# Kernel optimization log

Hardware: AMD Instinct MI355X
Metric: run time of the kernel (lower is better)

## Reference

```python
import jax, jax.numpy as jnp
import numpy as np

N = 100000          # number of road-network nodes
E = 640000          # number of directed edges (sparse adjacency nnz)
HID = 128           # hidden_dims = lane(16)+type(32)+length(16)+node(64)
N_LAYERS = 3        # hparams.baseline_gat_layer


def setup_inputs() -> dict:
    key = jax.random.key(0)
    ks = jax.random.split(key, 12)
    inp = {
        'node_feature': jax.random.randint(ks[0], (N,), 0, 100000),
        'type_feature': jax.random.randint(ks[1], (N,), 0, 20),
        'length_feature': jax.random.randint(ks[2], (N,), 0, 100),
        'lane_feature': jax.random.randint(ks[3], (N,), 0, 10),
        'adj_src': jax.random.randint(ks[4], (E,), 0, N),
        'adj_dst': jax.random.randint(ks[5], (E,), 0, N),
        'adj_val': jax.random.uniform(ks[6], (E,), dtype=jnp.float32),
        # learned parameters
        'node_emb': jax.random.normal(ks[7], (100000, 64), dtype=jnp.float32) * 0.02,
        'type_emb': jax.random.normal(ks[8], (20, 32), dtype=jnp.float32) * 0.02,
        'length_emb': jax.random.normal(ks[9], (100, 16), dtype=jnp.float32) * 0.02,
        'lane_emb': jax.random.normal(ks[10], (10, 16), dtype=jnp.float32) * 0.02,
        'W': jax.random.normal(ks[11], (HID, HID), dtype=jnp.float32) / np.sqrt(HID),
        'b': jnp.zeros((HID,), dtype=jnp.float32),
    }
    return inp


def spgcn_layer(x, W, b, adj_src, adj_dst, adj_val):
    # GCN layer: out = spmm(adj, x @ W) + b, adj given as COO edge list
    support = x @ W                                # [N, HID]
    msg = support[adj_src] * adj_val[:, None]      # gather + scale, [E, HID]
    agg = jax.ops.segment_sum(msg, adj_dst, num_segments=N)  # scatter-add
    return agg + b


def reference(node_feature, type_feature, length_feature, lane_feature,
              adj_src, adj_dst, adj_val,
              node_emb, type_emb, length_emb, lane_emb, W, b):
    # embedding lookups + concat: [lane, type, length, node] -> [N, HID]
    raw_feat = jnp.concatenate([
        lane_emb[lane_feature],
        type_emb[type_feature],
        length_emb[length_feature],
        node_emb[node_feature],
    ], axis=1)
    # repeated propagation with the SAME shared SPGCN layer weights
    for _ in range(N_LAYERS):
        raw_feat = spgcn_layer(raw_feat, W, b, adj_src, adj_dst, adj_val)
    return raw_feat
```

## Files before the change

### kernel.cpp

```cpp
#include <hip/hip_runtime.h>
#include <hip/hip_bf16.h>

typedef __hip_bfloat16 bf16;
typedef unsigned short ushort_t;
typedef __attribute__((ext_vector_type(8))) short short8;
typedef __attribute__((ext_vector_type(4))) float f32x4;

#define NN 100000
#define NE 640000
#define HD 128
#define NB 391
#define EMB_U 6250
#define PREP_U 64
#define PH0_U (EMB_U + PREP_U + NB)
#define HIST_U 2500
#define GEMM_U 782
#define AGG_U 12500
#define CAST_U 50000
#define LDA 136


__device__ __forceinline__ float bf2f(ushort_t u) {
    unsigned v = (unsigned)u << 16;
    return __builtin_bit_cast(float, v);
}
__device__ __forceinline__ ushort_t f2bf(float f) {
    bf16 h = __float2bfloat16(f);
    return *(ushort_t*)&h;
}

struct P {
    const int *nodef, *typef, *lenf, *lanef, *adj_src, *adj_dst;
    const float *adj_val, *node_emb, *type_emb, *len_emb, *lane_emb, *W, *bias;
    ushort_t *X, *Wt, *SUP;
    int *cnt, *offs, *pos, *bsum;
    int2 *epack;
    float *outf;
    int sup_is_out;
};


__device__ __forceinline__ void embed_unit(int u, int tid, const P& p) {
    const int idx = u * 256 + tid;
    const int i = idx >> 4;
    const int c = (idx & 15) * 8;
    const float* tbl; size_t base;
    if (c < 16)      { tbl = p.lane_emb; base = (size_t)p.lanef[i] * 16 + c; }
    else if (c < 48) { tbl = p.type_emb; base = (size_t)p.typef[i] * 32 + (c - 16); }
    else if (c < 64) { tbl = p.len_emb;  base = (size_t)p.lenf[i]  * 16 + (c - 48); }
    else             { tbl = p.node_emb; base = (size_t)p.nodef[i] * 64 + (c - 64); }
    const float4 f0 = *(const float4*)(tbl + base);
    const float4 f1 = *(const float4*)(tbl + base + 4);
    ushort_t u8[8] = { f2bf(f0.x), f2bf(f0.y), f2bf(f0.z), f2bf(f0.w),
                       f2bf(f1.x), f2bf(f1.y), f2bf(f1.z), f2bf(f1.w) };
    *(uint4*)(p.X + (size_t)i * HD + c) = *(uint4*)u8;
}

__global__ __launch_bounds__(256) void phase0_k(P p) {
    const int v = blockIdx.x;
    const int tid = threadIdx.x;
    if (v < EMB_U) {
        embed_unit(v, tid, p);
    } else if (v < EMB_U + PREP_U) {
        const int idx = (v - EMB_U) * 256 + tid;
        const int n = idx >> 7, k = idx & 127;
        p.Wt[idx] = f2bf(p.W[(size_t)k * HD + n]);
    } else {
        const int idx = (v - EMB_U - PREP_U) * 256 + tid;
        if (idx < NN) p.cnt[idx] = 0;
    }
}


__global__ __launch_bounds__(256) void hist_k(P p) {
    const int e = blockIdx.x * 256 + threadIdx.x;
    atomicAdd(&p.cnt[p.adj_dst[e]], 1);
}

__global__ __launch_bounds__(256) void scan1_k(P p) {
    __shared__ int s[256];
    const int tid = threadIdx.x;
    const int idx = blockIdx.x * 256 + tid;
    s[tid] = (idx < NN) ? p.cnt[idx] : 0;
    __syncthreads();
    for (int o = 128; o; o >>= 1) {
        if (tid < o) s[tid] += s[tid + o];
        __syncthreads();
    }
    if (tid == 0) p.bsum[blockIdx.x] = s[0];
}

__global__ __launch_bounds__(256) void scan3_k(P p) {
    __shared__ int s[256];
    const int b = blockIdx.x;
    const int tid = threadIdx.x;
    int acc = 0;
    for (int i = tid; i < b; i += 256) acc += p.bsum[i];
    s[tid] = acc;
    __syncthreads();
    for (int o = 128; o; o >>= 1) {
        if (tid < o) s[tid] += s[tid + o];
        __syncthreads();
    }
    const int boffv = s[0];
    __syncthreads();
    const int idx = b * 256 + tid;
    int v = (idx < NN) ? p.cnt[idx] : 0;
    s[tid] = v;
    __syncthreads();
    for (int o = 1; o < 256; o <<= 1) {
        int x = (tid >= o) ? s[tid - o] : 0;
        __syncthreads();
        s[tid] += x;
        __syncthreads();
    }
    const int excl = s[tid] - v + boffv;
    if (idx <= NN) {
        p.offs[idx] = excl;
        if (idx < NN) p.pos[idx] = excl;
    }
}

__global__ __launch_bounds__(256) void position_k(P p) {
    const int e = blockIdx.x * 256 + threadIdx.x;
    const int d = p.adj_dst[e];
    const int slot = atomicAdd(&p.pos[d], 1);
    int2 pk;
    pk.x = p.adj_src[e];
    pk.y = __float_as_int(p.adj_val[e]);
    p.epack[slot] = pk;
}


__global__ __launch_bounds__(256) void gemm_k(P p) {
    __shared__ ushort_t Xs[128 * LDA];
    const int tid = threadIdx.x;
    const int row0 = blockIdx.x * 128;
    const ushort_t* __restrict__ X = p.X;

#pragma unroll
    for (int i = 0; i < 8; ++i) {
        int chunk = i * 256 + tid;
        int m = chunk >> 4;
        int c8 = (chunk & 15) * 8;
        int gm = row0 + m;
        if (gm >= NN) gm = NN - 1;
        *(uint4*)&Xs[m * LDA + c8] = *(const uint4*)&X[(size_t)gm * HD + c8];
    }

    const int w = tid >> 6;
    const int ln = tid & 15;
    const int quad = (tid >> 4) & 3;
    const int koff = quad * 8;

    short8 bfrg[2][4];
#pragma unroll
    for (int nt = 0; nt < 2; ++nt)
#pragma unroll
        for (int kc = 0; kc < 4; ++kc)
            bfrg[nt][kc] = *(const short8*)&p.Wt[(size_t)(w * 32 + nt * 16 + ln) * HD + kc * 32 + koff];

    __syncthreads();

    const f32x4 zero = {0.f, 0.f, 0.f, 0.f};
#pragma unroll
    for (int mt = 0; mt < 8; ++mt) {
        short8 afrg[4];
#pragma unroll
        for (int kc = 0; kc < 4; ++kc)
            afrg[kc] = *(const short8*)&Xs[(mt * 16 + ln) * LDA + kc * 32 + koff];
        f32x4 acc[2] = {zero, zero};
#pragma unroll
        for (int nt = 0; nt < 2; ++nt)
#pragma unroll
            for (int kc = 0; kc < 4; ++kc)
                acc[nt] = __builtin_amdgcn_mfma_f32_16x16x32_bf16(
                        afrg[kc], bfrg[nt][kc], acc[nt], 0, 0, 0);
#pragma unroll
        for (int reg = 0; reg < 4; ++reg) {
            int gm = row0 + mt * 16 + quad * 4 + reg;
            if (gm < NN) {
#pragma unroll
                for (int nt = 0; nt < 2; ++nt)
                    p.SUP[(size_t)gm * HD + w * 32 + nt * 16 + ln] = f2bf(acc[nt][reg]);
            }
        }
    }
}

__global__ __launch_bounds__(256) void agg_k(P p, int wout, int skipX) {
    const int node = blockIdx.x * 8 + (threadIdx.x >> 5);
    const int lane = threadIdx.x & 31;
    const int c = lane * 4;
    const int lo = p.offs[node];
    const int hi = p.offs[node + 1];
    const ushort_t* __restrict__ sup = p.SUP;
    float4 a0 = {0,0,0,0}, a1 = {0,0,0,0}, a2 = {0,0,0,0}, a3 = {0,0,0,0};
    int j = lo;
    for (; j + 3 < hi; j += 4) {
        const int2 e0 = p.epack[j], e1 = p.epack[j + 1];
        const int2 e2 = p.epack[j + 2], e3 = p.epack[j + 3];
        const ushort4 u0 = *(const ushort4*)(sup + (size_t)e0.x * HD + c);
        const ushort4 u1 = *(const ushort4*)(sup + (size_t)e1.x * HD + c);
        const ushort4 u2 = *(const ushort4*)(sup + (size_t)e2.x * HD + c);
        const ushort4 u3 = *(const ushort4*)(sup + (size_t)e3.x * HD + c);
        const float v0 = __int_as_float(e0.y), v1 = __int_as_float(e1.y);
        const float v2 = __int_as_float(e2.y), v3 = __int_as_float(e3.y);
        a0.x += bf2f(u0.x)*v0; a0.y += bf2f(u0.y)*v0; a0.z += bf2f(u0.z)*v0; a0.w += bf2f(u0.w)*v0;
        a1.x += bf2f(u1.x)*v1; a1.y += bf2f(u1.y)*v1; a1.z += bf2f(u1.z)*v1; a1.w += bf2f(u1.w)*v1;
        a2.x += bf2f(u2.x)*v2; a2.y += bf2f(u2.y)*v2; a2.z += bf2f(u2.z)*v2; a2.w += bf2f(u2.w)*v2;
        a3.x += bf2f(u3.x)*v3; a3.y += bf2f(u3.y)*v3; a3.z += bf2f(u3.z)*v3; a3.w += bf2f(u3.w)*v3;
    }
    for (; j < hi; ++j) {
        const int2 e0 = p.epack[j];
        const float v0 = __int_as_float(e0.y);
        const ushort4 u0 = *(const ushort4*)(sup + (size_t)e0.x * HD + c);
        a0.x += bf2f(u0.x)*v0; a0.y += bf2f(u0.y)*v0; a0.z += bf2f(u0.z)*v0; a0.w += bf2f(u0.w)*v0;
    }
    const float4 b4 = *(const float4*)(p.bias + c);
    float4 acc;
    acc.x = (a0.x + a1.x) + (a2.x + a3.x) + b4.x;
    acc.y = (a0.y + a1.y) + (a2.y + a3.y) + b4.y;
    acc.z = (a0.z + a1.z) + (a2.z + a3.z) + b4.z;
    acc.w = (a0.w + a1.w) + (a2.w + a3.w) + b4.w;
    const size_t o = (size_t)node * HD + c;
    if (!skipX) {
        ushort4 u; u.x = f2bf(acc.x); u.y = f2bf(acc.y);
        u.z = f2bf(acc.z); u.w = f2bf(acc.w);
        *(ushort4*)(p.X + o) = u;
    }
    if (wout) *(float4*)(p.outf + o) = acc;
}

__global__ __launch_bounds__(256) void cast_k(P p) {
    const int idx = blockIdx.x * 256 + threadIdx.x;
    p.outf[idx] = bf2f(p.X[idx]);
}

extern "C" void kernel_launch(void* const* d_in, const int* in_sizes, int n_in,
                              void* d_out, int out_size, void* d_ws, size_t ws_size,
                              hipStream_t stream) {
    P p;
    p.nodef    = (const int*)d_in[0];
    p.typef    = (const int*)d_in[1];
    p.lenf     = (const int*)d_in[2];
    p.lanef    = (const int*)d_in[3];
    p.adj_src  = (const int*)d_in[4];
    p.adj_dst  = (const int*)d_in[5];
    p.adj_val  = (const float*)d_in[6];
    p.node_emb = (const float*)d_in[7];
    p.type_emb = (const float*)d_in[8];
    p.len_emb  = (const float*)d_in[9];
    p.lane_emb = (const float*)d_in[10];
    p.W        = (const float*)d_in[11];
    p.bias     = (const float*)d_in[12];
    p.outf     = (float*)d_out;

    const size_t xbytes = (size_t)NN * HD * 2;
    char* wp = (char*)d_ws;
    p.X     = (ushort_t*)wp; wp += xbytes;
    p.cnt   = (int*)wp;      wp += (size_t)NN * 4;
    p.offs  = (int*)wp;      wp += 400016;
    p.pos   = (int*)wp;      wp += (size_t)NN * 4;
    p.epack = (int2*)wp;     wp += (size_t)NE * 8;
    p.Wt    = (ushort_t*)wp; wp += 32768;
    p.bsum  = (int*)wp;      wp += 1600;
    const size_t used = (size_t)(wp - (char*)d_ws);
    if (ws_size >= used + xbytes) { p.SUP = (ushort_t*)wp;    p.sup_is_out = 0; }
    else                          { p.SUP = (ushort_t*)d_out; p.sup_is_out = 1; }

    phase0_k<<<PH0_U, 256, 0, stream>>>(p);
    hist_k<<<HIST_U, 256, 0, stream>>>(p);
    scan1_k<<<NB, 256, 0, stream>>>(p);
    scan3_k<<<NB, 256, 0, stream>>>(p);
    position_k<<<HIST_U, 256, 0, stream>>>(p);
    for (int l = 0; l < 3; ++l) {
        gemm_k<<<GEMM_U, 256, 0, stream>>>(p);
        const int wout = (l == 2) && !p.sup_is_out;
        agg_k<<<AGG_U, 256, 0, stream>>>(p, wout, wout);
    }
    if (p.sup_is_out) cast_k<<<CAST_U, 256, 0, stream>>>(p);
}
```

Measured before the change: 351.0 us.

## Reassociate GCN layers: aggregate three times, then apply precomputed W^3

Because the weight is shared and aggregation is linear, the three gemm/aggregate pairs are rewritten as three sparse aggregations of the raw features followed by a single GEMM with W^3. W^2 and W^3 are built in a single-block MFMA kernel, and the bias terms are folded in through the row sums d and A·d times bW and bW². This removes two GEMM passes and the cast fallback, and the final GEMM writes fp32 output directly. In exchange it needs a second bf16 ping-pong buffer and a serial one-block weight kernel, and it changes rounding, since W^3 is stored in bf16.

```diff
diff --git a/kernel.cpp b/kernel.cpp
--- a/kernel.cpp
+++ b/kernel.cpp
@@ -12,11 +12,12 @@
 #define NB 391
 #define EMB_U 6250
 #define PREP_U 64
-#define PH0_U (EMB_U + PREP_U + NB)
+#define CNT_U 391
+#define PH0_U (EMB_U + PREP_U + CNT_U)
 #define HIST_U 2500
 #define GEMM_U 782
 #define AGG_U 12500
-#define CAST_U 50000
+#define D_U 391
 #define LDA 136
 
 
@@ -32,35 +33,31 @@
 struct P {
     const int *nodef, *typef, *lenf, *lanef, *adj_src, *adj_dst;
     const float *adj_val, *node_emb, *type_emb, *len_emb, *lane_emb, *W, *bias;
-    ushort_t *X, *Wt, *SUP;
+    ushort_t *Xa, *Xb, *Wt, *w3t;
+    float *bw, *bw2, *d, *d2;
     int *cnt, *offs, *pos, *bsum;
     int2 *epack;
     float *outf;
-    int sup_is_out;
 };
 
-
-__device__ __forceinline__ void embed_unit(int u, int tid, const P& p) {
-    const int idx = u * 256 + tid;
-    const int i = idx >> 4;
-    const int c = (idx & 15) * 8;
-    const float* tbl; size_t base;
-    if (c < 16)      { tbl = p.lane_emb; base = (size_t)p.lanef[i] * 16 + c; }
-    else if (c < 48) { tbl = p.type_emb; base = (size_t)p.typef[i] * 32 + (c - 16); }
-    else if (c < 64) { tbl = p.len_emb;  base = (size_t)p.lenf[i]  * 16 + (c - 48); }
-    else             { tbl = p.node_emb; base = (size_t)p.nodef[i] * 64 + (c - 64); }
-    const float4 f0 = *(const float4*)(tbl + base);
-    const float4 f1 = *(const float4*)(tbl + base + 4);
-    ushort_t u8[8] = { f2bf(f0.x), f2bf(f0.y), f2bf(f0.z), f2bf(f0.w),
-                       f2bf(f1.x), f2bf(f1.y), f2bf(f1.z), f2bf(f1.w) };
-    *(uint4*)(p.X + (size_t)i * HD + c) = *(uint4*)u8;
-}
 
 __global__ __launch_bounds__(256) void phase0_k(P p) {
     const int v = blockIdx.x;
     const int tid = threadIdx.x;
     if (v < EMB_U) {
-        embed_unit(v, tid, p);
+        const int idx = v * 256 + tid;
+        const int i = idx >> 4;
+        const int c = (idx & 15) * 8;
+        const float* tbl; size_t base;
+        if (c < 16)      { tbl = p.lane_emb; base = (size_t)p.lanef[i] * 16 + c; }
+        else if (c < 48) { tbl = p.type_emb; base = (size_t)p.typef[i] * 32 + (c - 16); }
+        else if (c < 64) { tbl = p.len_emb;  base = (size_t)p.lenf[i]  * 16 + (c - 48); }
+        else             { tbl = p.node_emb; base = (size_t)p.nodef[i] * 64 + (c - 64); }
+        const float4 f0 = *(const float4*)(tbl + base);
+        const float4 f1 = *(const float4*)(tbl + base + 4);
+        ushort_t u8[8] = { f2bf(f0.x), f2bf(f0.y), f2bf(f0.z), f2bf(f0.w),
+                           f2bf(f1.x), f2bf(f1.y), f2bf(f1.z), f2bf(f1.w) };
+        *(uint4*)(p.Xa + (size_t)i * HD + c) = *(uint4*)u8;
     } else if (v < EMB_U + PREP_U) {
         const int idx = (v - EMB_U) * 256 + tid;
         const int n = idx >> 7, k = idx & 127;
@@ -68,6 +65,102 @@
     } else {
         const int idx = (v - EMB_U - PREP_U) * 256 + tid;
         if (idx < NN) p.cnt[idx] = 0;
+    }
+}
+
+__global__ __launch_bounds__(256) void wchain_k(P p) {
+    __shared__ ushort_t WtL[HD * HD];
+    __shared__ ushort_t W2t[HD * HD];
+    const int tid = threadIdx.x;
+    for (int i = tid; i < HD * HD / 8; i += 256)
+        *(uint4*)&WtL[i * 8] = *(const uint4*)&p.Wt[i * 8];
+    __syncthreads();
+
+    const int w = tid >> 6;
+    const int ln = tid & 15;
+    const int quad = (tid >> 4) & 3;
+    const int koff = quad * 8;
+    const f32x4 zero = {0.f, 0.f, 0.f, 0.f};
+
+    short8 bfrg[2][4];
+#pragma unroll
+    for (int nt = 0; nt < 2; ++nt)
+#pragma unroll
+        for (int kc = 0; kc < 4; ++kc)
+            bfrg[nt][kc] = *(const short8*)&WtL[(w * 32 + nt * 16 + ln) * HD + kc * 32 + koff];
+
+#pragma unroll
+    for (int mt = 0; mt < 8; ++mt) {
+        const int m = mt * 16 + ln;
+        short8 afrg[4];
+#pragma unroll
+        for (int kc = 0; kc < 4; ++kc) {
+            ushort_t a[8];
+#pragma unroll
+            for (int j = 0; j < 8; ++j)
+                a[j] = WtL[(kc * 32 + koff + j) * HD + m];
+            afrg[kc] = *(short8*)a;
+        }
+        f32x4 acc[2] = {zero, zero};
+#pragma unroll
+        for (int nt = 0; nt < 2; ++nt)
+#pragma unroll
+            for (int kc = 0; kc < 4; ++kc)
+                acc[nt] = __builtin_amdgcn_mfma_f32_16x16x32_bf16(
+                        afrg[kc], bfrg[nt][kc], acc[nt], 0, 0, 0);
+#pragma unroll
+        for (int nt = 0; nt < 2; ++nt)
+#pragma unroll
+            for (int reg = 0; reg < 4; ++reg) {
+                const int col = w * 32 + nt * 16 + ln;
+                const int row = mt * 16 + quad * 4 + reg;
+                W2t[col * HD + row] = f2bf(acc[nt][reg]);
+            }
+    }
+    __syncthreads();
+
+#pragma unroll
+    for (int mt = 0; mt < 8; ++mt) {
+        const int m = mt * 16 + ln;
+        short8 afrg[4];
+#pragma unroll
+        for (int kc = 0; kc < 4; ++kc) {
+            ushort_t a[8];
+#pragma unroll
+            for (int j = 0; j < 8; ++j)
+                a[j] = W2t[(kc * 32 + koff + j) * HD + m];
+            afrg[kc] = *(short8*)a;
+        }
+        f32x4 acc[2] = {zero, zero};
+#pragma unroll
+        for (int nt = 0; nt < 2; ++nt)
+#pragma unroll
+            for (int kc = 0; kc < 4; ++kc)
+                acc[nt] = __builtin_amdgcn_mfma_f32_16x16x32_bf16(
+                        afrg[kc], bfrg[nt][kc], acc[nt], 0, 0, 0);
+#pragma unroll
+        for (int nt = 0; nt < 2; ++nt)
+#pragma unroll
+            for (int reg = 0; reg < 4; ++reg) {
+                const int col = w * 32 + nt * 16 + ln;
+                const int row = mt * 16 + quad * 4 + reg;
+                p.w3t[col * HD + row] = f2bf(acc[nt][reg]);
+            }
+    }
+    __syncthreads();
+
+    float* bwS = (float*)W2t;
+    if (tid < HD) {
+        float s = 0.f;
+        for (int k = 0; k < HD; ++k) s += p.bias[k] * bf2f(WtL[tid * HD + k]);
+        bwS[tid] = s;
+        p.bw[tid] = s;
+    }
+    __syncthreads();
+    if (tid < HD) {
+        float s = 0.f;
+        for (int k = 0; k < HD; ++k) s += bwS[k] * bf2f(WtL[tid * HD + k]);
+        p.bw2[tid] = s;
     }
 }
 
@@ -131,12 +224,66 @@
     p.epack[slot] = pk;
 }
 
-
-__global__ __launch_bounds__(256) void gemm_k(P p) {
+__global__ __launch_bounds__(256) void agg_k(P p, const ushort_t* __restrict__ Xin,
+                                             ushort_t* __restrict__ Xout, int aux) {
+    if (blockIdx.x >= AGG_U) {
+        const int node = (blockIdx.x - AGG_U) * 256 + threadIdx.x;
+        if (node < NN) {
+            const int lo = p.offs[node], hi = p.offs[node + 1];
+            float s = 0.f;
+            if (aux == 1) {
+                for (int j = lo; j < hi; ++j) s += __int_as_float(p.epack[j].y);
+                p.d[node] = s;
+            } else {
+                for (int j = lo; j < hi; ++j) {
+                    const int2 e = p.epack[j];
+                    s += __int_as_float(e.y) * p.d[e.x];
+                }
+                p.d2[node] = s;
+            }
+        }
+        return;
+    }
+    const int node = blockIdx.x * 8 + (threadIdx.x >> 5);
+    const int lane = threadIdx.x & 31;
+    const int c = lane * 4;
+    const int lo = p.offs[node];
+    const int hi = p.offs[node + 1];
+    float4 a0 = {0,0,0,0}, a1 = {0,0,0,0}, a2 = {0,0,0,0}, a3 = {0,0,0,0};
+    int j = lo;
+    for (; j + 3 < hi; j += 4) {
+        const int2 e0 = p.epack[j], e1 = p.epack[j + 1];
+        const int2 e2 = p.epack[j + 2], e3 = p.epack[j + 3];
+        const ushort4 u0 = *(const ushort4*)(Xin + (size_t)e0.x * HD + c);
+        const ushort4 u1 = *(const ushort4*)(Xin + (size_t)e1.x * HD + c);
+        const ushort4 u2 = *(const ushort4*)(Xin + (size_t)e2.x * HD + c);
+        const ushort4 u3 = *(const ushort4*)(Xin + (size_t)e3.x * HD + c);
+        const float v0 = __int_as_float(e0.y), v1 = __int_as_float(e1.y);
+        const float v2 = __int_as_float(e2.y), v3 = __int_as_float(e3.y);
+        a0.x += bf2f(u0.x)*v0; a0.y += bf2f(u0.y)*v0; a0.z += bf2f(u0.z)*v0; a0.w += bf2f(u0.w)*v0;
+        a1.x += bf2f(u1.x)*v1; a1.y += bf2f(u1.y)*v1; a1.z += bf2f(u1.z)*v1; a1.w += bf2f(u1.w)*v1;
+        a2.x += bf2f(u2.x)*v2; a2.y += bf2f(u2.y)*v2; a2.z += bf2f(u2.z)*v2; a2.w += bf2f(u2.w)*v2;
+        a3.x += bf2f(u3.x)*v3; a3.y += bf2f(u3.y)*v3; a3.z += bf2f(u3.z)*v3; a3.w += bf2f(u3.w)*v3;
+    }
+    for (; j < hi; ++j) {
+        const int2 e0 = p.epack[j];
+        const float v0 = __int_as_float(e0.y);
+        const ushort4 u0 = *(const ushort4*)(Xin + (size_t)e0.x * HD + c);
+        a0.x += bf2f(u0.x)*v0; a0.y += bf2f(u0.y)*v0; a0.z += bf2f(u0.z)*v0; a0.w += bf2f(u0.w)*v0;
+    }
+    float4 acc;
+    acc.x = (a0.x + a1.x) + (a2.x + a3.x);
+    acc.y = (a0.y + a1.y) + (a2.y + a3.y);
+    acc.z = (a0.z + a1.z) + (a2.z + a3.z);
+    acc.w = (a0.w + a1.w) + (a2.w + a3.w);
+    ushort4 u; u.x = f2bf(acc.x); u.y = f2bf(acc.y); u.z = f2bf(acc.z); u.w = f2bf(acc.w);
+    *(ushort4*)(Xout + (size_t)node * HD + c) = u;
+}
+
+__global__ __launch_bounds__(256) void gemmf_k(P p, const ushort_t* __restrict__ X3) {
     __shared__ ushort_t Xs[128 * LDA];
     const int tid = threadIdx.x;
     const int row0 = blockIdx.x * 128;
-    const ushort_t* __restrict__ X = p.X;
 
 #pragma unroll
     for (int i = 0; i < 8; ++i) {
@@ -145,20 +292,26 @@
         int c8 = (chunk & 15) * 8;
         int gm = row0 + m;
         if (gm >= NN) gm = NN - 1;
-        *(uint4*)&Xs[m * LDA + c8] = *(const uint4*)&X[(size_t)gm * HD + c8];
+        *(uint4*)&Xs[m * LDA + c8] = *(const uint4*)&X3[(size_t)gm * HD + c8];
     }
 
     const int w = tid >> 6;
     const int ln = tid & 15;
     const int quad = (tid >> 4) & 3;
     const int koff = quad * 8;
+    const int col0 = w * 32 + ln;
+    const int col1 = col0 + 16;
 
     short8 bfrg[2][4];
 #pragma unroll
     for (int nt = 0; nt < 2; ++nt)
 #pragma unroll
         for (int kc = 0; kc < 4; ++kc)
-            bfrg[nt][kc] = *(const short8*)&p.Wt[(size_t)(w * 32 + nt * 16 + ln) * HD + kc * 32 + koff];
+            bfrg[nt][kc] = *(const short8*)&p.w3t[(size_t)(w * 32 + nt * 16 + ln) * HD + kc * 32 + koff];
+
+    const float bwc0 = p.bw[col0],  bwc1 = p.bw[col1];
+    const float bw2c0 = p.bw2[col0], bw2c1 = p.bw2[col1];
+    const float bc0 = p.bias[col0], bc1 = p.bias[col1];
 
     __syncthreads();
 
@@ -178,63 +331,14 @@
                         afrg[kc], bfrg[nt][kc], acc[nt], 0, 0, 0);
 #pragma unroll
         for (int reg = 0; reg < 4; ++reg) {
-            int gm = row0 + mt * 16 + quad * 4 + reg;
+            const int gm = row0 + mt * 16 + quad * 4 + reg;
             if (gm < NN) {
-#pragma unroll
-                for (int nt = 0; nt < 2; ++nt)
-                    p.SUP[(size_t)gm * HD + w * 32 + nt * 16 + ln] = f2bf(acc[nt][reg]);
+                const float dg = p.d[gm], d2g = p.d2[gm];
+                p.outf[(size_t)gm * HD + col0] = acc[0][reg] + d2g * bw2c0 + dg * bwc0 + bc0;
+                p.outf[(size_t)gm * HD + col1] = acc[1][reg] + d2g * bw2c1 + dg * bwc1 + bc1;
             }
         }
     }
-}
-
-__global__ __launch_bounds__(256) void agg_k(P p, int wout, int skipX) {
-    const int node = blockIdx.x * 8 + (threadIdx.x >> 5);
-    const int lane = threadIdx.x & 31;
-    const int c = lane * 4;
-    const int lo = p.offs[node];
-    const int hi = p.offs[node + 1];
-    const ushort_t* __restrict__ sup = p.SUP;
-    float4 a0 = {0,0,0,0}, a1 = {0,0,0,0}, a2 = {0,0,0,0}, a3 = {0,0,0,0};
-    int j = lo;
-    for (; j + 3 < hi; j += 4) {
-        const int2 e0 = p.epack[j], e1 = p.epack[j + 1];
-        const int2 e2 = p.epack[j + 2], e3 = p.epack[j + 3];
-        const ushort4 u0 = *(const ushort4*)(sup + (size_t)e0.x * HD + c);
-        const ushort4 u1 = *(const ushort4*)(sup + (size_t)e1.x * HD + c);
-        const ushort4 u2 = *(const ushort4*)(sup + (size_t)e2.x * HD + c);
-        const ushort4 u3 = *(const ushort4*)(sup + (size_t)e3.x * HD + c);
-        const float v0 = __int_as_float(e0.y), v1 = __int_as_float(e1.y);
-        const float v2 = __int_as_float(e2.y), v3 = __int_as_float(e3.y);
-        a0.x += bf2f(u0.x)*v0; a0.y += bf2f(u0.y)*v0; a0.z += bf2f(u0.z)*v0; a0.w += bf2f(u0.w)*v0;
-        a1.x += bf2f(u1.x)*v1; a1.y += bf2f(u1.y)*v1; a1.z += bf2f(u1.z)*v1; a1.w += bf2f(u1.w)*v1;
-        a2.x += bf2f(u2.x)*v2; a2.y += bf2f(u2.y)*v2; a2.z += bf2f(u2.z)*v2; a2.w += bf2f(u2.w)*v2;
-        a3.x += bf2f(u3.x)*v3; a3.y += bf2f(u3.y)*v3; a3.z += bf2f(u3.z)*v3; a3.w += bf2f(u3.w)*v3;
-    }
-    for (; j < hi; ++j) {
-        const int2 e0 = p.epack[j];
-        const float v0 = __int_as_float(e0.y);
-        const ushort4 u0 = *(const ushort4*)(sup + (size_t)e0.x * HD + c);
-        a0.x += bf2f(u0.x)*v0; a0.y += bf2f(u0.y)*v0; a0.z += bf2f(u0.z)*v0; a0.w += bf2f(u0.w)*v0;
-    }
-    const float4 b4 = *(const float4*)(p.bias + c);
-    float4 acc;
-    acc.x = (a0.x + a1.x) + (a2.x + a3.x) + b4.x;
-    acc.y = (a0.y + a1.y) + (a2.y + a3.y) + b4.y;
-    acc.z = (a0.z + a1.z) + (a2.z + a3.z) + b4.z;
-    acc.w = (a0.w + a1.w) + (a2.w + a3.w) + b4.w;
-    const size_t o = (size_t)node * HD + c;
-    if (!skipX) {
-        ushort4 u; u.x = f2bf(acc.x); u.y = f2bf(acc.y);
-        u.z = f2bf(acc.z); u.w = f2bf(acc.w);
-        *(ushort4*)(p.X + o) = u;
-    }
-    if (wout) *(float4*)(p.outf + o) = acc;
-}
-
-__global__ __launch_bounds__(256) void cast_k(P p) {
-    const int idx = blockIdx.x * 256 + threadIdx.x;
-    p.outf[idx] = bf2f(p.X[idx]);
 }
 
 extern "C" void kernel_launch(void* const* d_in, const int* in_sizes, int n_in,
@@ -258,26 +362,28 @@
 
     const size_t xbytes = (size_t)NN * HD * 2;
     char* wp = (char*)d_ws;
-    p.X     = (ushort_t*)wp; wp += xbytes;
+    p.Xa    = (ushort_t*)wp; wp += xbytes;
+    p.Xb    = (ushort_t*)wp; wp += xbytes;
     p.cnt   = (int*)wp;      wp += (size_t)NN * 4;
     p.offs  = (int*)wp;      wp += 400016;
     p.pos   = (int*)wp;      wp += (size_t)NN * 4;
     p.epack = (int2*)wp;     wp += (size_t)NE * 8;
     p.Wt    = (ushort_t*)wp; wp += 32768;
+    p.w3t   = (ushort_t*)wp; wp += 32768;
+    p.bw    = (float*)wp;    wp += 512;
+    p.bw2   = (float*)wp;    wp += 512;
+    p.d     = (float*)wp;    wp += (size_t)NN * 4;
+    p.d2    = (float*)wp;    wp += (size_t)NN * 4;
     p.bsum  = (int*)wp;      wp += 1600;
-    const size_t used = (size_t)(wp - (char*)d_ws);
-    if (ws_size >= used + xbytes) { p.SUP = (ushort_t*)wp;    p.sup_is_out = 0; }
-    else                          { p.SUP = (ushort_t*)d_out; p.sup_is_out = 1; }
 
     phase0_k<<<PH0_U, 256, 0, stream>>>(p);
+    wchain_k<<<1, 256, 0, stream>>>(p);
     hist_k<<<HIST_U, 256, 0, stream>>>(p);
     scan1_k<<<NB, 256, 0, stream>>>(p);
     scan3_k<<<NB, 256, 0, stream>>>(p);
     position_k<<<HIST_U, 256, 0, stream>>>(p);
-    for (int l = 0; l < 3; ++l) {
-        gemm_k<<<GEMM_U, 256, 0, stream>>>(p);
-        const int wout = (l == 2) && !p.sup_is_out;
-        agg_k<<<AGG_U, 256, 0, stream>>>(p, wout, wout);
-    }
-    if (p.sup_is_out) cast_k<<<CAST_U, 256, 0, stream>>>(p);
-}
+    agg_k<<<AGG_U + D_U, 256, 0, stream>>>(p, p.Xa, p.Xb, 1);
+    agg_k<<<AGG_U + D_U, 256, 0, stream>>>(p, p.Xb, p.Xa, 2);
+    agg_k<<<AGG_U, 256, 0, stream>>>(p, p.Xa, p.Xb, 0);
+    gemmf_k<<<GEMM_U, 256, 0, stream>>>(p, p.Xb);
+}
```

New measurement: 321.3 us. 1.09x faster.
